# Kernel tuning notes

Hardware: AMD Instinct MI355X
Metric: run time of the kernel (lower is better)

## Reference

```python
import jax, jax.numpy as jnp
import numpy as np

T, IN, H, L, OUT = 131072, 60, 14, 3, 7


def setup_inputs() -> dict:
    key = jax.random.key(0)
    ks = jax.random.split(key, 18)
    s = 1.0 / np.sqrt(H)  # torch default LSTM/Linear init scale
    u = lambda k, shp: jax.random.uniform(k, shp, jnp.float32, -s, s)
    return {
        "x": jax.random.normal(ks[0], (T, IN), jnp.float32),
        "h0": jax.random.uniform(ks[1], (L, H), jnp.float32),
        "c0": jax.random.uniform(ks[2], (L, H), jnp.float32),
        "W_ih0": u(ks[3], (4 * H, IN)), "W_hh0": u(ks[4], (4 * H, H)),
        "b_ih0": u(ks[5], (4 * H,)), "b_hh0": u(ks[6], (4 * H,)),
        "W_ih1": u(ks[7], (4 * H, H)), "W_hh1": u(ks[8], (4 * H, H)),
        "b_ih1": u(ks[9], (4 * H,)), "b_hh1": u(ks[10], (4 * H,)),
        "W_ih2": u(ks[11], (4 * H, H)), "W_hh2": u(ks[12], (4 * H, H)),
        "b_ih2": u(ks[13], (4 * H,)), "b_hh2": u(ks[14], (4 * H,)),
        "W_lin": u(ks[15], (OUT, H)), "b_lin": u(ks[16], (OUT,)),
    }


def _cell(xp, h, c, Whh, bhh):
    # PyTorch gate order: i, f, g, o
    g = xp + h @ Whh.T + bhh  # [4H]
    i, f, gg, o = jnp.split(g, 4, axis=-1)
    c = jax.nn.sigmoid(f) * c + jax.nn.sigmoid(i) * jnp.tanh(gg)
    h = jax.nn.sigmoid(o) * jnp.tanh(c)
    return h, c


def reference(x, h0, c0, W_ih0, W_hh0, b_ih0, b_hh0,
              W_ih1, W_hh1, b_ih1, b_hh1,
              W_ih2, W_hh2, b_ih2, b_hh2, W_lin, b_lin):
    # precompute layer-0 input projection (only GEMM that parallelizes over T)
    xw0 = x @ W_ih0.T + b_ih0  # [T, 4H]

    def step(carry, xp):
        h, c = carry  # [L, H] each
        h0n, c0n = _cell(xp, h[0], c[0], W_hh0, b_hh0)
        h1n, c1n = _cell(h0n @ W_ih1.T + b_ih1, h[1], c[1], W_hh1, b_hh1)
        h2n, c2n = _cell(h1n @ W_ih2.T + b_ih2, h[2], c[2], W_hh2, b_hh2)
        return (jnp.stack([h0n, h1n, h2n]), jnp.stack([c0n, c1n, c2n])), h2n

    _, out = jax.lax.scan(step, (h0, c0), xw0)  # out: [T, H]
    return jax.nn.relu(jax.nn.relu(out) @ W_lin.T + b_lin)  # [T, OUT]
```

## Files before the change

kernel.cpp:

```cpp
#include <hip/hip_runtime.h>

#define T_TOT 131072
#define IN_DIM 60
#define H_DIM 14
#define G4 56
#define OUT_DIM 7
#define S_CHUNK 32
#define N_CHUNK (T_TOT / S_CHUNK)
#define WARM 32
#define LOG2E 1.44269504088896340736f
#define LSTRIDE 33

__device__ __forceinline__ float frcp(float x)  { return __builtin_amdgcn_rcpf(x); }
__device__ __forceinline__ float fexp2(float x) { return __builtin_amdgcn_exp2f(x); }
__device__ __forceinline__ float rlane(float v, int l) {
    return __int_as_float(__builtin_amdgcn_readlane(__float_as_int(v), l));
}
__device__ __forceinline__ float bperm(int addr, float v) {
    return __int_as_float(__builtin_amdgcn_ds_bpermute(addr, __float_as_int(v)));
}

__global__ __launch_bounds__(64)
void prep(const float* __restrict__ Wih0, const float* __restrict__ bih0,
          const float* __restrict__ bhh0, float* __restrict__ WT)
{
    const int i = threadIdx.x;
    for (int idx = i; idx < IN_DIM * G4; idx += 64) {
        const int k = idx / G4, j = idx % G4;
        const float sc = (j >= 28 && j < 42) ? -2.f * LOG2E : -LOG2E;
        WT[idx] = Wih0[j * IN_DIM + k] * sc;
    }
    if (i < G4) {
        const float sc = (i >= 28 && i < 42) ? -2.f * LOG2E : -LOG2E;
        WT[IN_DIM * G4 + i] = (bih0[i] + bhh0[i]) * sc;
    }
}

__global__ __attribute__((amdgpu_flat_work_group_size(256, 256), amdgpu_waves_per_eu(2, 2)))
void xproj(const float* __restrict__ x, const float* __restrict__ WT,
           float* __restrict__ xw0)
{
    const int t = blockIdx.x * 256 + threadIdx.x;
    float xr[IN_DIM];
    const float4* xrow = (const float4*)(x + (size_t)t * IN_DIM);
#pragma unroll
    for (int i = 0; i < IN_DIM / 4; ++i) {
        const float4 v = xrow[i];
        xr[4 * i] = v.x; xr[4 * i + 1] = v.y; xr[4 * i + 2] = v.z; xr[4 * i + 3] = v.w;
    }
    float acc[G4];
#pragma unroll
    for (int j = 0; j < G4; ++j) acc[j] = WT[IN_DIM * G4 + j];
#pragma unroll 2
    for (int k = 0; k < IN_DIM; ++k) {
        const float xk = xr[k];
#pragma unroll
        for (int j = 0; j < G4; ++j) acc[j] = fmaf(xk, WT[k * G4 + j], acc[j]);
    }
    float4* orow = (float4*)(xw0 + (size_t)t * G4);
#pragma unroll
    for (int j = 0; j < G4 / 4; ++j)
        orow[j] = (float4){acc[4 * j], acc[4 * j + 1], acc[4 * j + 2], acc[4 * j + 3]};
}

__global__ __attribute__((amdgpu_flat_work_group_size(64, 64), amdgpu_waves_per_eu(4, 4)))
void lstm_fused(const float* __restrict__ xw0,
                const float* __restrict__ Whh0,
                const float* __restrict__ Wih1, const float* __restrict__ Whh1,
                const float* __restrict__ Wih2, const float* __restrict__ Whh2,
                const float* __restrict__ bih1, const float* __restrict__ bhh1,
                const float* __restrict__ bih2, const float* __restrict__ bhh2,
                const float* __restrict__ h0in, const float* __restrict__ c0in,
                const float* __restrict__ Wlin, const float* __restrict__ blin,
                float* __restrict__ out)
{
    __shared__ float stash[S_CHUNK * LSTRIDE];

    const int lane = threadIdx.x;
    const int j = lane < G4 ? lane : G4 - 1;
    const float sc = (j >= 28 && j < 42) ? -2.f * LOG2E : -LOG2E;

    float w0[H_DIM], wi1[H_DIM], wh1[H_DIM], wi2[H_DIM], wh2[H_DIM];
#pragma unroll
    for (int k = 0; k < H_DIM; ++k) {
        w0[k]  = Whh0[j * H_DIM + k] * sc;
        wi1[k] = Wih1[j * H_DIM + k] * sc;
        wh1[k] = Whh1[j * H_DIM + k] * sc;
        wi2[k] = Wih2[j * H_DIM + k] * sc;
        wh2[k] = Whh2[j * H_DIM + k] * sc;
    }
    const float bias1 = (bih1[j] + bhh1[j]) * sc;
    const float bias2 = (bih2[j] + bhh2[j]) * sc;

    const bool  isG  = (lane >= 28 && lane < 42);
    const float amul = isG ?  2.f :  1.f;
    const float aadd = isG ? -1.f :  0.f;

    const int aF = ((lane + 14) & 63) << 2;
    const int aG = ((lane + 28) & 63) << 2;
    const int aO = ((lane + 42) & 63) << 2;

    const int t0 = blockIdx.x * S_CHUNK;
    int start = t0 - WARM;
    float h0v, c0v, h1v, c1v, h2v, c2v;
    const int sl = lane < H_DIM ? lane : 0;
    int ug1, ug2;
    if (start <= 0) {
        start = 0;
        h0v = h0in[sl]; h1v = h0in[H_DIM + sl]; h2v = h0in[2 * H_DIM + sl];
        c0v = c0in[sl]; c1v = c0in[H_DIM + sl]; c2v = c0in[2 * H_DIM + sl];
        ug1 = 1; ug2 = 2;
    } else {
        h0v = h1v = h2v = 0.f; c0v = c1v = c2v = 0.f;
        ug1 = start; ug2 = start;
    }
    const int tend = t0 + S_CHUNK;

    const float* xp = xw0 + (size_t)start * G4 + j;
    float xv  = xp[0];
    float xn1 = xp[G4];

    auto step = [&](int u, bool gated, bool store_en) {
        const float xn2 = xp[2 * G4];

        float g0a = xv,    g0b = 0.f;
        float g1a = bias1, g1b = 0.f, g1c = 0.f, g1d = 0.f;
        float g2a = bias2, g2b = 0.f, g2c = 0.f, g2d = 0.f;
#pragma unroll
        for (int k = 0; k < 7; ++k) {
            const float s0a = rlane(h0v, k), s0b = rlane(h0v, k + 7);
            const float s1a = rlane(h1v, k), s1b = rlane(h1v, k + 7);
            const float s2a = rlane(h2v, k), s2b = rlane(h2v, k + 7);
            g0a = fmaf(s0a, w0[k],      g0a);
            g0b = fmaf(s0b, w0[k + 7],  g0b);
            g1a = fmaf(s0a, wi1[k],     g1a);
            g1b = fmaf(s0b, wi1[k + 7], g1b);
            g1c = fmaf(s1a, wh1[k],     g1c);
            g1d = fmaf(s1b, wh1[k + 7], g1d);
            g2a = fmaf(s1a, wi2[k],     g2a);
            g2b = fmaf(s1b, wi2[k + 7], g2b);
            g2c = fmaf(s2a, wh2[k],     g2c);
            g2d = fmaf(s2b, wh2[k + 7], g2d);
        }
        const float a0 = fmaf(amul, frcp(1.f + fexp2(g0a + g0b)), aadd);
        const float a1 = fmaf(amul, frcp(1.f + fexp2((g1a + g1b) + (g1c + g1d))), aadd);
        const float a2 = fmaf(amul, frcp(1.f + fexp2((g2a + g2b) + (g2c + g2d))), aadd);

        {
            const float fv = bperm(aF, a0), gv = bperm(aG, a0), ov = bperm(aO, a0);
            const float cn = fmaf(fv, c0v, a0 * gv);
            const float th = fmaf(2.f, frcp(1.f + fexp2(-2.f * LOG2E * cn)), -1.f);
            c0v = cn; h0v = ov * th;
        }
        if (!gated || u >= ug1) {
            const float fv = bperm(aF, a1), gv = bperm(aG, a1), ov = bperm(aO, a1);
            const float cn = fmaf(fv, c1v, a1 * gv);
            const float th = fmaf(2.f, frcp(1.f + fexp2(-2.f * LOG2E * cn)), -1.f);
            c1v = cn; h1v = ov * th;
        }
        if (!gated || u >= ug2) {
            const float fv = bperm(aF, a2), gv = bperm(aG, a2), ov = bperm(aO, a2);
            const float cn = fmaf(fv, c2v, a2 * gv);
            const float th = fmaf(2.f, frcp(1.f + fexp2(-2.f * LOG2E * cn)), -1.f);
            c2v = cn; h2v = ov * th;
            if (store_en)
                stash[(u - 2 - t0) * LSTRIDE + lane] = h2v;
        }
        xv = xn1; xn1 = xn2; xp += G4;
    };

    for (int u = start; u < t0; ++u)        step(u, false, false);
    step(t0,     true, false);
    step(t0 + 1, true, false);
    for (int u = t0 + 2; u < tend + 2; ++u) step(u, false, true);

    __syncthreads();
    if (lane < S_CHUNK) {
        float h[H_DIM];
#pragma unroll
        for (int k = 0; k < H_DIM; ++k) {
            const float v = stash[lane * LSTRIDE + k];
            h[k] = v > 0.f ? v : 0.f;
        }
        float* orow = out + (size_t)(t0 + lane) * OUT_DIM;
#pragma unroll
        for (int o = 0; o < OUT_DIM; ++o) {
            float acc = blin[o];
#pragma unroll
            for (int k = 0; k < H_DIM; ++k) acc = fmaf(h[k], Wlin[o * H_DIM + k], acc);
            orow[o] = acc > 0.f ? acc : 0.f;
        }
    }
}

extern "C" void kernel_launch(void* const* d_in, const int* in_sizes, int n_in,
                              void* d_out, int out_size, void* d_ws, size_t ws_size,
                              hipStream_t stream)
{
    const float* x     = (const float*)d_in[0];
    const float* h0    = (const float*)d_in[1];
    const float* c0    = (const float*)d_in[2];
    const float* W_ih0 = (const float*)d_in[3];
    const float* W_hh0 = (const float*)d_in[4];
    const float* b_ih0 = (const float*)d_in[5];
    const float* b_hh0 = (const float*)d_in[6];
    const float* W_ih1 = (const float*)d_in[7];
    const float* W_hh1 = (const float*)d_in[8];
    const float* b_ih1 = (const float*)d_in[9];
    const float* b_hh1 = (const float*)d_in[10];
    const float* W_ih2 = (const float*)d_in[11];
    const float* W_hh2 = (const float*)d_in[12];
    const float* b_ih2 = (const float*)d_in[13];
    const float* b_hh2 = (const float*)d_in[14];
    const float* W_lin = (const float*)d_in[15];
    const float* b_lin = (const float*)d_in[16];
    float* out = (float*)d_out;

    float* xw0 = (float*)d_ws;
    float* WT  = xw0 + (size_t)(T_TOT + 4) * G4;

    prep<<<1, 64, 0, stream>>>(W_ih0, b_ih0, b_hh0, WT);
    xproj<<<T_TOT / 256, 256, 0, stream>>>(x, WT, xw0);
    lstm_fused<<<N_CHUNK, 64, 0, stream>>>(xw0, W_hh0, W_ih1, W_hh1, W_ih2, W_hh2,
                                           b_ih1, b_hh1, b_ih2, b_hh2, h0, c0,
                                           W_lin, b_lin, out);
}
```

Before: 224.8 us.

## Double LSTM chunk size and restructure warmup loop with 4-deep x prefetch

Each block now handles 64 timesteps instead of 32, with 34 warmup steps, which halves the block count and lowers the fraction of redundant warmup recurrence. The per-step lambda is split into gate and cell helpers, the gating special case is confined to block 0, and the other blocks run a 4-step unrolled loop with four-deep prefetch of the input projection. The occupancy hint is lowered to two waves per EU. In exchange each block runs a longer serial chain, and fewer waves are available to hide latency.

```diff
diff --git a/kernel.cpp b/kernel.cpp
--- a/kernel.cpp
+++ b/kernel.cpp
@@ -5,11 +5,11 @@
 #define H_DIM 14
 #define G4 56
 #define OUT_DIM 7
-#define S_CHUNK 32
+#define S_CHUNK 64
 #define N_CHUNK (T_TOT / S_CHUNK)
-#define WARM 32
+#define WARM 34
 #define LOG2E 1.44269504088896340736f
-#define LSTRIDE 33
+#define LSTRIDE 65
 
 __device__ __forceinline__ float frcp(float x)  { return __builtin_amdgcn_rcpf(x); }
 __device__ __forceinline__ float fexp2(float x) { return __builtin_amdgcn_exp2f(x); }
@@ -63,7 +63,7 @@
         orow[j] = (float4){acc[4 * j], acc[4 * j + 1], acc[4 * j + 2], acc[4 * j + 3]};
 }
 
-__global__ __attribute__((amdgpu_flat_work_group_size(64, 64), amdgpu_waves_per_eu(4, 4)))
+__global__ __attribute__((amdgpu_flat_work_group_size(64, 64), amdgpu_waves_per_eu(2, 2)))
 void lstm_fused(const float* __restrict__ xw0,
                 const float* __restrict__ Whh0,
                 const float* __restrict__ Wih1, const float* __restrict__ Whh1,
@@ -101,28 +101,10 @@
     const int aO = ((lane + 42) & 63) << 2;
 
     const int t0 = blockIdx.x * S_CHUNK;
-    int start = t0 - WARM;
     float h0v, c0v, h1v, c1v, h2v, c2v;
-    const int sl = lane < H_DIM ? lane : 0;
-    int ug1, ug2;
-    if (start <= 0) {
-        start = 0;
-        h0v = h0in[sl]; h1v = h0in[H_DIM + sl]; h2v = h0in[2 * H_DIM + sl];
-        c0v = c0in[sl]; c1v = c0in[H_DIM + sl]; c2v = c0in[2 * H_DIM + sl];
-        ug1 = 1; ug2 = 2;
-    } else {
-        h0v = h1v = h2v = 0.f; c0v = c1v = c2v = 0.f;
-        ug1 = start; ug2 = start;
-    }
-    const int tend = t0 + S_CHUNK;
-
-    const float* xp = xw0 + (size_t)start * G4 + j;
-    float xv  = xp[0];
-    float xn1 = xp[G4];
-
-    auto step = [&](int u, bool gated, bool store_en) {
-        const float xn2 = xp[2 * G4];
-
+    int saddr = lane;
+
+    auto gates = [&](float xv, float& a0, float& a1, float& a2) {
         float g0a = xv,    g0b = 0.f;
         float g1a = bias1, g1b = 0.f, g1c = 0.f, g1d = 0.f;
         float g2a = bias2, g2b = 0.f, g2c = 0.f, g2d = 0.f;
@@ -142,54 +124,85 @@
             g2c = fmaf(s2a, wh2[k],     g2c);
             g2d = fmaf(s2b, wh2[k + 7], g2d);
         }
-        const float a0 = fmaf(amul, frcp(1.f + fexp2(g0a + g0b)), aadd);
-        const float a1 = fmaf(amul, frcp(1.f + fexp2((g1a + g1b) + (g1c + g1d))), aadd);
-        const float a2 = fmaf(amul, frcp(1.f + fexp2((g2a + g2b) + (g2c + g2d))), aadd);
-
+        a0 = fmaf(amul, frcp(1.f + fexp2(g0a + g0b)), aadd);
+        a1 = fmaf(amul, frcp(1.f + fexp2((g1a + g1b) + (g1c + g1d))), aadd);
+        a2 = fmaf(amul, frcp(1.f + fexp2((g2a + g2b) + (g2c + g2d))), aadd);
+    };
+    auto cellupd = [&](float a, float& cv) -> float {
+        const float fv = bperm(aF, a), gv = bperm(aG, a), ov = bperm(aO, a);
+        const float cn = fmaf(fv, cv, a * gv);
+        const float th = fmaf(2.f, frcp(1.f + fexp2(-2.f * LOG2E * cn)), -1.f);
+        cv = cn;
+        return ov * th;
+    };
+    auto step = [&](float xv, bool store_en) {
+        float a0, a1, a2;
+        gates(xv, a0, a1, a2);
+        h0v = cellupd(a0, c0v);
+        h1v = cellupd(a1, c1v);
+        h2v = cellupd(a2, c2v);
+        if (store_en) { stash[saddr] = h2v; saddr += LSTRIDE; }
+    };
+
+    if (blockIdx.x == 0) {
+        const int sl = lane < H_DIM ? lane : 0;
+        h0v = h0in[sl]; h1v = h0in[H_DIM + sl]; h2v = h0in[2 * H_DIM + sl];
+        c0v = c0in[sl]; c1v = c0in[H_DIM + sl]; c2v = c0in[2 * H_DIM + sl];
+        const float* xp = xw0 + j;
+        float xv = xp[0], xn1 = xp[G4];
         {
-            const float fv = bperm(aF, a0), gv = bperm(aG, a0), ov = bperm(aO, a0);
-            const float cn = fmaf(fv, c0v, a0 * gv);
-            const float th = fmaf(2.f, frcp(1.f + fexp2(-2.f * LOG2E * cn)), -1.f);
-            c0v = cn; h0v = ov * th;
-        }
-        if (!gated || u >= ug1) {
-            const float fv = bperm(aF, a1), gv = bperm(aG, a1), ov = bperm(aO, a1);
-            const float cn = fmaf(fv, c1v, a1 * gv);
-            const float th = fmaf(2.f, frcp(1.f + fexp2(-2.f * LOG2E * cn)), -1.f);
-            c1v = cn; h1v = ov * th;
-        }
-        if (!gated || u >= ug2) {
-            const float fv = bperm(aF, a2), gv = bperm(aG, a2), ov = bperm(aO, a2);
-            const float cn = fmaf(fv, c2v, a2 * gv);
-            const float th = fmaf(2.f, frcp(1.f + fexp2(-2.f * LOG2E * cn)), -1.f);
-            c2v = cn; h2v = ov * th;
-            if (store_en)
-                stash[(u - 2 - t0) * LSTRIDE + lane] = h2v;
-        }
-        xv = xn1; xn1 = xn2; xp += G4;
-    };
-
-    for (int u = start; u < t0; ++u)        step(u, false, false);
-    step(t0,     true, false);
-    step(t0 + 1, true, false);
-    for (int u = t0 + 2; u < tend + 2; ++u) step(u, false, true);
+            float a0, a1, a2; gates(xv, a0, a1, a2);
+            h0v = cellupd(a0, c0v);
+            xv = xn1; xn1 = xp[2 * G4]; xp += G4;
+        }
+        {
+            float a0, a1, a2; gates(xv, a0, a1, a2);
+            h0v = cellupd(a0, c0v);
+            h1v = cellupd(a1, c1v);
+            xv = xn1; xn1 = xp[2 * G4]; xp += G4;
+        }
+#pragma unroll 1
+        for (int m = 0; m < S_CHUNK; ++m) {
+            step(xv, true);
+            xv = xn1; xn1 = xp[2 * G4]; xp += G4;
+        }
+    } else {
+        h0v = h1v = h2v = 0.f; c0v = c1v = c2v = 0.f;
+        const float* xp = xw0 + (size_t)(t0 - WARM) * G4 + j;
+        float x0 = xp[0], x1 = xp[G4], x2 = xp[2 * G4], x3 = xp[3 * G4];
+        xp += 4 * G4;
+#pragma unroll 1
+        for (int m = 0; m < (WARM + 2) / 4; ++m) {
+            step(x0, false); x0 = xp[0];
+            step(x1, false); x1 = xp[G4];
+            step(x2, false); x2 = xp[2 * G4];
+            step(x3, false); x3 = xp[3 * G4];
+            xp += 4 * G4;
+        }
+#pragma unroll 1
+        for (int m = 0; m < S_CHUNK / 4; ++m) {
+            step(x0, true); x0 = xp[0];
+            step(x1, true); x1 = xp[G4];
+            step(x2, true); x2 = xp[2 * G4];
+            step(x3, true); x3 = xp[3 * G4];
+            xp += 4 * G4;
+        }
+    }
 
     __syncthreads();
-    if (lane < S_CHUNK) {
-        float h[H_DIM];
-#pragma unroll
-        for (int k = 0; k < H_DIM; ++k) {
-            const float v = stash[lane * LSTRIDE + k];
-            h[k] = v > 0.f ? v : 0.f;
-        }
-        float* orow = out + (size_t)(t0 + lane) * OUT_DIM;
-#pragma unroll
-        for (int o = 0; o < OUT_DIM; ++o) {
-            float acc = blin[o];
-#pragma unroll
-            for (int k = 0; k < H_DIM; ++k) acc = fmaf(h[k], Wlin[o * H_DIM + k], acc);
-            orow[o] = acc > 0.f ? acc : 0.f;
-        }
+    float h[H_DIM];
+#pragma unroll
+    for (int k = 0; k < H_DIM; ++k) {
+        const float v = stash[lane * LSTRIDE + k];
+        h[k] = v > 0.f ? v : 0.f;
+    }
+    float* orow = out + (size_t)(t0 + lane) * OUT_DIM;
+#pragma unroll
+    for (int o = 0; o < OUT_DIM; ++o) {
+        float acc = blin[o];
+#pragma unroll
+        for (int k = 0; k < H_DIM; ++k) acc = fmaf(h[k], Wlin[o * H_DIM + k], acc);
+        orow[o] = acc > 0.f ? acc : 0.f;
     }
 }
 
@@ -217,7 +230,7 @@
     float* out = (float*)d_out;
 
     float* xw0 = (float*)d_ws;
-    float* WT  = xw0 + (size_t)(T_TOT + 4) * G4;
+    float* WT  = xw0 + (size_t)(T_TOT + 8) * G4;
 
     prep<<<1, 64, 0, stream>>>(W_ih0, b_ih0, b_hh0, WT);
     xproj<<<T_TOT / 256, 256, 0, stream>>>(x, WT, xw0);
```

Result: faster. 203.9 us (-9.3%).
